# Kernel optimization log

Hardware: AMD Instinct MI355X
Metric: run time of the kernel (lower is better)

Reference implementation:

```python
import jax, jax.numpy as jnp
import numpy as np

DIM = 768
H = 4
D_H = DIM // H          # 192
R_H = 16 // H           # 4  (max(1, rank//num_heads))
N_EXP = 6
TOPK = 3
BETA = 0.5
BATCH = 65536


def setup_inputs() -> dict:
    key = jax.random.key(0)
    k_z, k_a, k_b, k_zs, k_za = jax.random.split(key, 5)
    z = jax.random.normal(k_z, (BATCH, DIM), dtype=jnp.float32)
    A = jax.random.normal(k_a, (N_EXP, D_H, R_H), dtype=jnp.float32) * 0.02
    B = jax.random.normal(k_b, (N_EXP, R_H, D_H), dtype=jnp.float32) * 0.02
    Z_share = jax.random.normal(k_zs, (H, N_EXP), dtype=jnp.float32) * 0.02
    Z_auth = jax.random.normal(k_za, (H, N_EXP), dtype=jnp.float32) * 0.02
    return {"z": z, "A": A, "B": B, "Z_share": Z_share, "Z_auth": Z_auth}


def _route(z_heads, Z_router, A, B):
    # z_heads: [Bt, h, d_h]; Z_router: [h, E]
    probs = jax.nn.softmax(Z_router, axis=-1)            # [h, E]
    top_vals, top_idx = jax.lax.top_k(probs, TOPK)       # [h, k]
    w = top_vals / (jnp.sum(top_vals, axis=-1, keepdims=True) + 1e-8)  # renorm per head
    A_g = A[top_idx]                                     # [h, k, d_h, r_h]
    B_g = B[top_idx]                                     # [h, k, r_h, d_h]
    # tmp[b,h,k,r] = z[b,h,:] @ A_g[h,k]
    tmp = jnp.einsum('bhd,hkdr->bhkr', z_heads, A_g)
    delta = jnp.einsum('bhkr,hkrd,hk->bhd', tmp, B_g, w)
    return delta


def reference(z, A, B, Z_share, Z_auth):
    Bt = z.shape[0]
    z_heads = z.reshape(Bt, H, D_H)
    delta = _route(z_heads, Z_share, A, B) + _route(z_heads, Z_auth, A, B)
    return z + BETA * delta.reshape(Bt, DIM)
```

## Files before the change

kernel.cpp:

```cpp
#include <hip/hip_runtime.h>
#include <hip/hip_bf16.h>


typedef float f4 __attribute__((ext_vector_type(4)));

__global__ void dff_setup(const float* __restrict__ A,
                          const float* __restrict__ Zs,
                          const float* __restrict__ Za,
                          float* __restrict__ Ac) {
  __shared__ float c[4][6];
  const int t = threadIdx.x;
  if (t < 4) {
    const int h = t;
    float cc[6] = {0.f, 0.f, 0.f, 0.f, 0.f, 0.f};
    for (int rt = 0; rt < 2; ++rt) {
      const float* Z = rt ? Za : Zs;
      float zz[6];
      float mx = -1e30f;
      for (int e = 0; e < 6; ++e) { zz[e] = Z[h * 6 + e]; mx = fmaxf(mx, zz[e]); }
      float p[6];
      float sum = 0.f;
      for (int e = 0; e < 6; ++e) { p[e] = expf(zz[e] - mx); sum += p[e]; }
      for (int e = 0; e < 6; ++e) p[e] /= sum;
      bool used[6] = {false, false, false, false, false, false};
      float ws = 0.f;
      int sel[3];
      float pv[3];
      for (int k = 0; k < 3; ++k) {
        int best = -1;
        float bv = -1.f;
        for (int e = 0; e < 6; ++e)
          if (!used[e] && p[e] > bv) { bv = p[e]; best = e; }
        used[best] = true;
        sel[k] = best;
        pv[k] = bv;
        ws += bv;
      }
      const float inv = 1.f / (ws + 1e-8f);
      for (int k = 0; k < 3; ++k) cc[sel[k]] += pv[k] * inv;
    }
    for (int e = 0; e < 6; ++e) c[h][e] = 0.5f * cc[e];
  }
  __syncthreads();
  for (int idx = threadIdx.x; idx < 4 * 24 * 192; idx += blockDim.x) {
    const int h = idx / (24 * 192);
    const int rem = idx % (24 * 192);
    const int s = rem / 192;
    const int d = rem % 192;
    const int e = s >> 2, r = s & 3;
    Ac[idx] = c[h][e] * A[e * 768 + d * 4 + r];
  }
}

__global__ __launch_bounds__(256, 4)
void dff_main(const float* __restrict__ z,
              const float* __restrict__ B,
              const float* __restrict__ Ac,
              float* __restrict__ out) {
  __shared__ float sA[24 * 192];
  __shared__ float sB[24 * 192];

  const int t = threadIdx.x;
  const int q = t & 7;
  const int rl = t >> 3;
  const int h = blockIdx.y;
  const int row = blockIdx.x * 32 + rl;
  const float* __restrict__ zp = z + (size_t)row * 768 + h * 192;
  float* __restrict__ op = out + (size_t)row * 768 + h * 192;

  f4 zv[6];
#pragma unroll
  for (int j = 0; j < 6; ++j)
    zv[j] = __builtin_nontemporal_load(reinterpret_cast<const f4*>(zp) + 8 * j + q);

  {
    const f4* __restrict__ Ag = reinterpret_cast<const f4*>(Ac + h * (24 * 192));
    const f4* __restrict__ Bg = reinterpret_cast<const f4*>(B);
    f4* sAv = reinterpret_cast<f4*>(sA);
    f4* sBv = reinterpret_cast<f4*>(sB);
    for (int i = t; i < 1152; i += 256) {
      sAv[i] = Ag[i];
      sBv[i] = Bg[i];
    }
  }
  __syncthreads();

  float tmp[24];
#pragma unroll
  for (int s = 0; s < 24; ++s) tmp[s] = 0.f;

#pragma unroll
  for (int j = 0; j < 6; ++j) {
    const int d0 = (8 * j + q) * 4;
#pragma unroll
    for (int s = 0; s < 24; ++s) {
      const f4 a = *reinterpret_cast<const f4*>(sA + s * 192 + d0);
      tmp[s] = fmaf(zv[j].x, a.x,
               fmaf(zv[j].y, a.y,
               fmaf(zv[j].z, a.z,
               fmaf(zv[j].w, a.w, tmp[s]))));
    }
  }

#pragma unroll
  for (int s = 0; s < 24; ++s) {
    tmp[s] += __shfl_xor(tmp[s], 1, 64);
    tmp[s] += __shfl_xor(tmp[s], 2, 64);
    tmp[s] += __shfl_xor(tmp[s], 4, 64);
  }

#pragma unroll
  for (int j = 0; j < 6; ++j) {
    const int d0 = (8 * j + q) * 4;
    f4 o = zv[j];
#pragma unroll
    for (int s = 0; s < 24; ++s) {
      const f4 b = *reinterpret_cast<const f4*>(sB + s * 192 + d0);
      const float tv = tmp[s];
      o.x = fmaf(tv, b.x, o.x);
      o.y = fmaf(tv, b.y, o.y);
      o.z = fmaf(tv, b.z, o.z);
      o.w = fmaf(tv, b.w, o.w);
    }
    __builtin_nontemporal_store(o, reinterpret_cast<f4*>(op) + 8 * j + q);
  }
}

extern "C" void kernel_launch(void* const* d_in, const int* in_sizes, int n_in,
                              void* d_out, int out_size, void* d_ws, size_t ws_size,
                              hipStream_t stream) {
  const float* z  = (const float*)d_in[0];
  const float* A  = (const float*)d_in[1];
  const float* B  = (const float*)d_in[2];
  const float* Zs = (const float*)d_in[3];
  const float* Za = (const float*)d_in[4];
  float* out = (float*)d_out;
  float* Ac = (float*)d_ws;

  dff_setup<<<1, 256, 0, stream>>>(A, Zs, Za, Ac);
  dff_main<<<dim3(2048, 4), 256, 0, stream>>>(z, B, Ac, out);
}
```

Measured before the change: 124.1 us.

## Use packed bf16 dot2 for both low-rank projections with repacked weights

The setup kernel now packs the scaled A weights and the B weights into bf16 pairs. The main kernel converts z to bf16 pairs and uses the fdot2 instruction for both the down-projection and the up-projection. This halves the shared-memory footprint and LDS traffic and roughly halves the FMA count. In exchange, z and the intermediate values lose precision to bf16 rounding, and z is now read twice from global memory: once with plain loads for packing and again for the residual add.

```diff
diff --git a/kernel.cpp b/kernel.cpp
--- a/kernel.cpp
+++ b/kernel.cpp
@@ -3,11 +3,36 @@
 
 
 typedef float f4 __attribute__((ext_vector_type(4)));
+typedef unsigned int u32;
+typedef u32 u32x4 __attribute__((ext_vector_type(4)));
+
+__device__ __forceinline__ u32 pack_bf16(float a, float b) {
+  const u32 ua = __builtin_bit_cast(u32, a) + 0x8000u;
+  const u32 ub = __builtin_bit_cast(u32, b) + 0x8000u;
+  return (ua >> 16) | (ub & 0xFFFF0000u);
+}
+
+#if __has_builtin(__builtin_amdgcn_fdot2_f32_bf16)
+typedef __bf16 bf16x2 __attribute__((ext_vector_type(2)));
+__device__ __forceinline__ float dot2(u32 a, u32 b, float c) {
+  return __builtin_amdgcn_fdot2_f32_bf16(__builtin_bit_cast(bf16x2, a),
+                                         __builtin_bit_cast(bf16x2, b), c, false);
+}
+#else
+__device__ __forceinline__ float dot2(u32 a, u32 b, float c) {
+  const float alo = __builtin_bit_cast(float, a << 16);
+  const float ahi = __builtin_bit_cast(float, a & 0xFFFF0000u);
+  const float blo = __builtin_bit_cast(float, b << 16);
+  const float bhi = __builtin_bit_cast(float, b & 0xFFFF0000u);
+  return fmaf(ahi, bhi, fmaf(alo, blo, c));
+}
+#endif
 
 __global__ void dff_setup(const float* __restrict__ A,
+                          const float* __restrict__ Bm,
                           const float* __restrict__ Zs,
                           const float* __restrict__ Za,
-                          float* __restrict__ Ac) {
+                          u32* __restrict__ T) {
   __shared__ float c[4][6];
   const int t = threadIdx.x;
   if (t < 4) {
@@ -42,23 +67,31 @@
     for (int e = 0; e < 6; ++e) c[h][e] = 0.5f * cc[e];
   }
   __syncthreads();
-  for (int idx = threadIdx.x; idx < 4 * 24 * 192; idx += blockDim.x) {
-    const int h = idx / (24 * 192);
-    const int rem = idx % (24 * 192);
-    const int s = rem / 192;
-    const int d = rem % 192;
-    const int e = s >> 2, r = s & 3;
-    Ac[idx] = c[h][e] * A[e * 768 + d * 4 + r];
+  for (int i = threadIdx.x; i < 11520; i += blockDim.x) {
+    if (i < 9216) {
+      const int h = i / 2304;
+      const int rem = i % 2304;
+      const int s = rem / 96;
+      const int dp = rem % 96;
+      const int e = s >> 2, r = s & 3;
+      const float lo = c[h][e] * A[e * 768 + (2 * dp) * 4 + r];
+      const float hi = c[h][e] * A[e * 768 + (2 * dp + 1) * 4 + r];
+      T[i] = pack_bf16(lo, hi);
+    } else {
+      const int k = i - 9216;
+      const int sp = k / 192;
+      const int d = k % 192;
+      T[i] = pack_bf16(Bm[(2 * sp) * 192 + d], Bm[(2 * sp + 1) * 192 + d]);
+    }
   }
 }
 
 __global__ __launch_bounds__(256, 4)
 void dff_main(const float* __restrict__ z,
-              const float* __restrict__ B,
-              const float* __restrict__ Ac,
+              const u32* __restrict__ T,
               float* __restrict__ out) {
-  __shared__ float sA[24 * 192];
-  __shared__ float sB[24 * 192];
+  __shared__ __align__(16) u32 sT[4608];
+  u32x4* sT4 = reinterpret_cast<u32x4*>(sT);
 
   const int t = threadIdx.x;
   const int q = t & 7;
@@ -70,36 +103,40 @@
 
   f4 zv[6];
 #pragma unroll
-  for (int j = 0; j < 6; ++j)
-    zv[j] = __builtin_nontemporal_load(reinterpret_cast<const f4*>(zp) + 8 * j + q);
+  for (int k = 0; k < 6; ++k)
+    zv[k] = reinterpret_cast<const f4*>(zp)[16 * (k >> 1) + 2 * q + (k & 1)];
 
   {
-    const f4* __restrict__ Ag = reinterpret_cast<const f4*>(Ac + h * (24 * 192));
-    const f4* __restrict__ Bg = reinterpret_cast<const f4*>(B);
-    f4* sAv = reinterpret_cast<f4*>(sA);
-    f4* sBv = reinterpret_cast<f4*>(sB);
-    for (int i = t; i < 1152; i += 256) {
-      sAv[i] = Ag[i];
-      sBv[i] = Bg[i];
+    const u32x4* __restrict__ Tw = reinterpret_cast<const u32x4*>(T);
+    for (int i = t; i < 576; i += 256) {
+      sT4[i] = Tw[h * 576 + i];
+      sT4[576 + i] = Tw[2304 + i];
     }
+  }
+
+  u32 zpk[12];
+#pragma unroll
+  for (int j = 0; j < 3; ++j) {
+    zpk[4 * j + 0] = pack_bf16(zv[2 * j].x, zv[2 * j].y);
+    zpk[4 * j + 1] = pack_bf16(zv[2 * j].z, zv[2 * j].w);
+    zpk[4 * j + 2] = pack_bf16(zv[2 * j + 1].x, zv[2 * j + 1].y);
+    zpk[4 * j + 3] = pack_bf16(zv[2 * j + 1].z, zv[2 * j + 1].w);
   }
   __syncthreads();
 
   float tmp[24];
 #pragma unroll
-  for (int s = 0; s < 24; ++s) tmp[s] = 0.f;
-
+  for (int s = 0; s < 24; ++s) {
+    float acc = 0.f;
 #pragma unroll
-  for (int j = 0; j < 6; ++j) {
-    const int d0 = (8 * j + q) * 4;
-#pragma unroll
-    for (int s = 0; s < 24; ++s) {
-      const f4 a = *reinterpret_cast<const f4*>(sA + s * 192 + d0);
-      tmp[s] = fmaf(zv[j].x, a.x,
-               fmaf(zv[j].y, a.y,
-               fmaf(zv[j].z, a.z,
-               fmaf(zv[j].w, a.w, tmp[s]))));
+    for (int j = 0; j < 3; ++j) {
+      const u32x4 av = sT4[s * 24 + 8 * j + q];
+      acc = dot2(zpk[4 * j + 0], av.x, acc);
+      acc = dot2(zpk[4 * j + 1], av.y, acc);
+      acc = dot2(zpk[4 * j + 2], av.z, acc);
+      acc = dot2(zpk[4 * j + 3], av.w, acc);
     }
+    tmp[s] = acc;
   }
 
 #pragma unroll
@@ -109,20 +146,31 @@
     tmp[s] += __shfl_xor(tmp[s], 4, 64);
   }
 
+  u32 tp[12];
 #pragma unroll
-  for (int j = 0; j < 6; ++j) {
-    const int d0 = (8 * j + q) * 4;
-    f4 o = zv[j];
+  for (int i = 0; i < 12; ++i) tp[i] = pack_bf16(tmp[2 * i], tmp[2 * i + 1]);
+
 #pragma unroll
-    for (int s = 0; s < 24; ++s) {
-      const f4 b = *reinterpret_cast<const f4*>(sB + s * 192 + d0);
-      const float tv = tmp[s];
-      o.x = fmaf(tv, b.x, o.x);
-      o.y = fmaf(tv, b.y, o.y);
-      o.z = fmaf(tv, b.z, o.z);
-      o.w = fmaf(tv, b.w, o.w);
+  for (int j = 0; j < 3; ++j) {
+    const int c0 = 16 * j + 2 * q;
+    f4 o0 = reinterpret_cast<const f4*>(zp)[c0];
+    f4 o1 = reinterpret_cast<const f4*>(zp)[c0 + 1];
+#pragma unroll
+    for (int sp = 0; sp < 12; ++sp) {
+      const int base = 576 + sp * 48 + (8 * j + q) * 2;
+      const u32x4 b0 = sT4[base];
+      const u32x4 b1 = sT4[base + 1];
+      o0.x = dot2(tp[sp], b0.x, o0.x);
+      o0.y = dot2(tp[sp], b0.y, o0.y);
+      o0.z = dot2(tp[sp], b0.z, o0.z);
+      o0.w = dot2(tp[sp], b0.w, o0.w);
+      o1.x = dot2(tp[sp], b1.x, o1.x);
+      o1.y = dot2(tp[sp], b1.y, o1.y);
+      o1.z = dot2(tp[sp], b1.z, o1.z);
+      o1.w = dot2(tp[sp], b1.w, o1.w);
     }
-    __builtin_nontemporal_store(o, reinterpret_cast<f4*>(op) + 8 * j + q);
+    __builtin_nontemporal_store(o0, reinterpret_cast<f4*>(op) + c0);
+    __builtin_nontemporal_store(o1, reinterpret_cast<f4*>(op) + c0 + 1);
   }
 }
 
@@ -131,12 +179,12 @@
                               hipStream_t stream) {
   const float* z  = (const float*)d_in[0];
   const float* A  = (const float*)d_in[1];
-  const float* B  = (const float*)d_in[2];
+  const float* Bm = (const float*)d_in[2];
   const float* Zs = (const float*)d_in[3];
   const float* Za = (const float*)d_in[4];
   float* out = (float*)d_out;
-  float* Ac = (float*)d_ws;
+  u32* T = (u32*)d_ws;
 
-  dff_setup<<<1, 256, 0, stream>>>(A, Zs, Za, Ac);
-  dff_main<<<dim3(2048, 4), 256, 0, stream>>>(z, B, Ac, out);
+  dff_setup<<<1, 256, 0, stream>>>(A, Bm, Zs, Za, T);
+  dff_main<<<dim3(2048, 4), 256, 0, stream>>>(z, T, out);
 }
```

Result: slower. 133.1 us (+7.3%).
